# Kernel tuning notes

Hardware: AMD Instinct MI355X
Metric: run time of the kernel (lower is better)

The kernel has to match this reference:

```python
import jax, jax.numpy as jnp
import numpy as np

D_MODEL = 2048
NUM_HEADS = 16
D_H = D_MODEL // NUM_HEADS
D_LATENT = 512
B, S = 2, 2048


def setup_inputs() -> dict:
    key = jax.random.key(0)
    ks = jax.random.split(key, 10)
    sd = lambda fan_in: 1.0 / np.sqrt(fan_in)
    x = jax.random.normal(ks[0], (B, S, D_MODEL), dtype=jnp.float32)
    # weights stored as [in, out] so y = x @ W + b (same math as nn.Linear)
    w_latent = jax.random.uniform(ks[1], (D_MODEL, D_LATENT), jnp.float32, -sd(D_MODEL), sd(D_MODEL))
    b_latent = jax.random.uniform(ks[2], (D_LATENT,), jnp.float32, -sd(D_MODEL), sd(D_MODEL))
    w_q = jax.random.uniform(ks[3], (D_MODEL, D_MODEL), jnp.float32, -sd(D_MODEL), sd(D_MODEL))
    b_q = jax.random.uniform(ks[4], (D_MODEL,), jnp.float32, -sd(D_MODEL), sd(D_MODEL))
    # per-head K/V projections batched into [H, d_latent, d_h]
    w_k = jax.random.uniform(ks[5], (NUM_HEADS, D_LATENT, D_H), jnp.float32, -sd(D_LATENT), sd(D_LATENT))
    b_k = jax.random.uniform(ks[6], (NUM_HEADS, D_H), jnp.float32, -sd(D_LATENT), sd(D_LATENT))
    w_v = jax.random.uniform(ks[7], (NUM_HEADS, D_LATENT, D_H), jnp.float32, -sd(D_LATENT), sd(D_LATENT))
    b_v = jax.random.uniform(ks[8], (NUM_HEADS, D_H), jnp.float32, -sd(D_LATENT), sd(D_LATENT))
    w_o = jax.random.uniform(ks[9], (D_MODEL, D_MODEL), jnp.float32, -sd(D_MODEL), sd(D_MODEL))
    b_o = jnp.zeros((D_MODEL,), jnp.float32)
    return {"x": x, "w_latent": w_latent, "b_latent": b_latent, "w_q": w_q, "b_q": b_q,
            "w_k": w_k, "b_k": b_k, "w_v": w_v, "b_v": b_v, "w_o": w_o, "b_o": b_o}


def reference(x, w_latent, b_latent, w_q, b_q, w_k, b_k, w_v, b_v, w_o, b_o):
    batch, seq, d = x.shape
    # latent KV compression: [B,S,d_latent]
    z = x @ w_latent + b_latent
    # queries: [B,H,S,d_h]
    q = (x @ w_q + b_q).reshape(batch, seq, NUM_HEADS, D_H).transpose(0, 2, 1, 3)
    # per-head K/V projections fused into one batched GEMM: [B,H,S,d_h]
    k = jnp.einsum('bsl,hld->bhsd', z, w_k) + b_k[None, :, None, :]
    v = jnp.einsum('bsl,hld->bhsd', z, w_v) + b_v[None, :, None, :]
    attn = jnp.einsum('bhqd,bhkd->bhqk', q, k) / np.sqrt(D_H).astype(np.float32)
    attn = jax.nn.softmax(attn, axis=-1)
    out = jnp.einsum('bhqk,bhkd->bhqd', attn, v)          # [B,H,S,d_h]
    out = out.transpose(0, 2, 1, 3).reshape(batch, seq, d)  # [B,S,D]
    return out @ w_o + b_o
```

## Files before the change

kernel.cpp:

```cpp
#include <hip/hip_runtime.h>
#include <hip/hip_bf16.h>

#define H_ATT   16
#define DH      128
#define DMODEL  2048
#define DLAT    512
#define NB      2
#define SEQ     2048
#define MROWS   (NB * SEQ)
#define NQZ     (DMODEL + DLAT)
#define NKV     (2 * DMODEL)

#define SCL2 0.12751744f

typedef __bf16          bf16x8_t __attribute__((ext_vector_type(8)));
typedef float           f32x4_t  __attribute__((ext_vector_type(4)));
typedef unsigned short  u16x4_t  __attribute__((ext_vector_type(4)));

#if __has_builtin(__builtin_amdgcn_exp2f)
#define EXP2F(x) __builtin_amdgcn_exp2f(x)
#else
#define EXP2F(x) exp2f(x)
#endif

__device__ __forceinline__ unsigned short f2bf_u16(float f) {
  union { __bf16 b; unsigned short u; } cv; cv.b = (__bf16)f; return cv.u;
}

__device__ __forceinline__ void async_copy16(const __bf16* g, __bf16* l) {
  __builtin_amdgcn_global_load_lds(
      (const __attribute__((address_space(1))) unsigned int*)g,
      (__attribute__((address_space(3))) unsigned int*)l, 16, 0, 0);
}

#define NB_CAST 8192
#define NB_WQ   4096
#define NB_WL   1024
#define NB_WK   1024
#define NB_WV   1024
#define NB_WO   4096
#define NB_BIAS 26
#define NB_PREP (NB_CAST + NB_WQ + NB_WL + NB_WK + NB_WV + NB_WO + NB_BIAS)

__global__ void prep(const float* __restrict__ x,
                     const float* __restrict__ w_q, const float* __restrict__ w_latent,
                     const float* __restrict__ w_k, const float* __restrict__ w_v,
                     const float* __restrict__ w_o,
                     const float* __restrict__ b_q, const float* __restrict__ b_lat,
                     const float* __restrict__ b_k, const float* __restrict__ b_v,
                     __bf16* __restrict__ xb, __bf16* __restrict__ wqzt,
                     __bf16* __restrict__ wkvt, __bf16* __restrict__ wot,
                     float* __restrict__ bqz, float* __restrict__ bkv) {
  __shared__ float tile[32][33];
  int bi = blockIdx.x;
  int t  = threadIdx.x;

  if (bi < NB_CAST) {
    int i = bi * 256 + t;
    float4 v = ((const float4*)x)[i];
    ushort4 o;
    o.x = f2bf_u16(v.x); o.y = f2bf_u16(v.y); o.z = f2bf_u16(v.z); o.w = f2bf_u16(v.w);
    ((ushort4*)xb)[i] = o;
    return;
  }
  bi -= NB_CAST;

  const float* in = nullptr; __bf16* out = nullptr;
  int R = 0, C = 0, bx = 0, by = 0; float scale = 1.f;
  if (bi < NB_WQ) {
    in = w_q; out = wqzt; R = DMODEL; C = DMODEL; scale = SCL2;
    bx = bi & 63; by = bi >> 6;
  } else if ((bi -= NB_WQ) < NB_WL) {
    in = w_latent; out = wqzt + (size_t)DMODEL * DMODEL; R = DMODEL; C = DLAT;
    bx = bi & 15; by = bi >> 4;
  } else if ((bi -= NB_WL) < NB_WK) {
    int h = bi >> 6, rem = bi & 63;
    in = w_k + (size_t)h * DLAT * DH; out = wkvt + (size_t)h * DH * DLAT;
    R = DLAT; C = DH; bx = rem & 3; by = rem >> 2;
  } else if ((bi -= NB_WK) < NB_WV) {
    int h = bi >> 6, rem = bi & 63;
    in = w_v + (size_t)h * DLAT * DH;
    out = wkvt + (size_t)DMODEL * DLAT + (size_t)h * DH * DLAT;
    R = DLAT; C = DH; bx = rem & 3; by = rem >> 2;
  } else if ((bi -= NB_WV) < NB_WO) {
    in = w_o; out = wot; R = DMODEL; C = DMODEL;
    bx = bi & 63; by = bi >> 6;
  } else {
    bi -= NB_WO;
    int idx = bi * 256 + t;
    if (idx < DMODEL)                bqz[idx] = b_q[idx] * SCL2;
    else if (idx < NQZ)              bqz[idx] = b_lat[idx - DMODEL];
    else if (idx < NQZ + DMODEL)     bkv[idx - NQZ] = b_k[idx - NQZ];
    else if (idx < NQZ + NKV)        bkv[idx - NQZ] = b_v[idx - NQZ - DMODEL];
    return;
  }

  int tx = t & 31, ty = t >> 5;
  const float* ip = in + (size_t)(by * 32) * C + bx * 32;
  #pragma unroll
  for (int i = 0; i < 4; ++i)
    tile[ty + i * 8][tx] = ip[(size_t)(ty + i * 8) * C + tx];
  __syncthreads();
  __bf16* op = out + (size_t)(bx * 32) * R + by * 32;
  #pragma unroll
  for (int i = 0; i < 4; ++i)
    op[(size_t)(ty + i * 8) * R + tx] = (__bf16)(tile[tx][ty + i * 8] * scale);
}

#define BM 128
#define BN 128
#define BK 32

__device__ __forceinline__ void storec(float*  p, float v) { *p = v; }
__device__ __forceinline__ void storec(__bf16* p, float v) { *p = (__bf16)v; }

template <typename OutT, bool KVDUAL>
__global__ __launch_bounds__(256, 2)
void gemm_bt(const __bf16* __restrict__ A, const __bf16* __restrict__ Bt,
             const float* __restrict__ bias, OutT* __restrict__ C,
             __bf16* __restrict__ Cvt,
             int M, int N, int K, int lda, int ldc) {
  __shared__ __align__(16) __bf16 As[BM * BK];
  __shared__ __align__(16) __bf16 Bs[BN * BK];
  const int t    = threadIdx.x;
  const int wave = t >> 6, lane = t & 63;
  const int quad = lane >> 4, l16 = lane & 15;
  const int wm = (wave >> 1) * 64, wn = (wave & 1) * 64;
  const int row0 = blockIdx.y * BM, col0 = blockIdx.x * BN;
  const int srow = t >> 2, skc = t & 3;

  const __bf16* Ag  = A  + (size_t)(row0 + srow)      * lda + skc * 8;
  const __bf16* Ag2 = A  + (size_t)(row0 + srow + 64) * lda + skc * 8;
  const __bf16* Bg  = Bt + (size_t)(col0 + srow)      * K   + skc * 8;
  const __bf16* Bg2 = Bt + (size_t)(col0 + srow + 64) * K   + skc * 8;
  __bf16* Al  = As + t * 8;
  __bf16* Al2 = As + 2048 + t * 8;
  __bf16* Bl  = Bs + t * 8;
  __bf16* Bl2 = Bs + 2048 + t * 8;

  f32x4_t acc[4][4] = {};

  for (int k0 = 0; k0 < K; k0 += BK) {
    async_copy16(Ag  + k0, Al);
    async_copy16(Ag2 + k0, Al2);
    async_copy16(Bg  + k0, Bl);
    async_copy16(Bg2 + k0, Bl2);
    __syncthreads();
    bf16x8_t af[4], bfr[4];
    #pragma unroll
    for (int i = 0; i < 4; ++i)
      af[i] = *(const bf16x8_t*)(As + (wm + i * 16 + l16) * BK + quad * 8);
    #pragma unroll
    for (int j = 0; j < 4; ++j)
      bfr[j] = *(const bf16x8_t*)(Bs + (wn + j * 16 + l16) * BK + quad * 8);
    #pragma unroll
    for (int i = 0; i < 4; ++i)
      #pragma unroll
      for (int j = 0; j < 4; ++j)
        acc[i][j] = __builtin_amdgcn_mfma_f32_16x16x32_bf16(af[i], bfr[j], acc[i][j], 0, 0, 0);
    __syncthreads();
  }

  const bool vmode = KVDUAL && (col0 >= DMODEL);
  #pragma unroll
  for (int j = 0; j < 4; ++j) {
    int col = col0 + wn + j * 16 + l16;
    float bj = bias[col];
    #pragma unroll
    for (int i = 0; i < 4; ++i) {
      int row = row0 + wm + i * 16 + quad * 4;
      if (vmode) {
        u16x4_t pw;
        #pragma unroll
        for (int r = 0; r < 4; ++r) pw[r] = f2bf_u16(acc[i][j][r] + bj);
        size_t bb = (size_t)(row >> 11);
        int s = row & (SEQ - 1);
        *(u16x4_t*)(Cvt + bb * ((size_t)DMODEL * SEQ) + (size_t)(col - DMODEL) * SEQ + s) = pw;
      } else {
        #pragma unroll
        for (int r = 0; r < 4; ++r)
          storec(&C[(size_t)(row + r) * ldc + col], acc[i][j][r] + bj);
      }
    }
  }
}

#define TQ 128
#define TK 32

__global__ __launch_bounds__(256, 2)
void mla_attn(const __bf16* __restrict__ Qm, const __bf16* __restrict__ Km,
              const __bf16* __restrict__ Vtg, __bf16* __restrict__ Om) {
  __shared__ __align__(16) __bf16 Kls[2][8 * 512];
  __shared__ __align__(16) __bf16 Vls[3][8 * 512];
  __shared__ __align__(16) __bf16 Ps [2][8 * 512];
  __shared__ float Lbuf[2][TQ];

  const int t    = threadIdx.x;
  const int wave = t >> 6, lane = t & 63;
  const int quad = lane >> 4, l16 = lane & 15;
  const int wq = wave >> 1, wk = wave & 1, wd = wave & 1;
  const int h = blockIdx.y, b = blockIdx.z;
  const int q0 = blockIdx.x * TQ;
  const size_t kbase  = (size_t)b * SEQ * DMODEL + (size_t)h * DH;
  const size_t vtbase = ((size_t)b * DMODEL + (size_t)h * DH) * SEQ;
  const size_t obase  = (size_t)b * SEQ * DMODEL + (size_t)h * DH;

  bf16x8_t qf[4][4];
  #pragma unroll
  for (int nt = 0; nt < 4; ++nt) {
    const __bf16* qp = Qm + ((size_t)b * SEQ + q0 + wq * 64 + nt * 16 + l16) * NQZ
                       + (size_t)h * DH + quad * 8;
    #pragma unroll
    for (int kc = 0; kc < 4; ++kc)
      qf[nt][kc] = *(const bf16x8_t*)(qp + kc * 32);
  }

  auto stage = [&](int tile) {
    int kt0 = tile * TK;
    __bf16* Kd = Kls[tile & 1];
    __bf16* Vd = Vls[tile % 3];
    #pragma unroll
    for (int i2 = 0; i2 < 2; ++i2) {
      int bidx = wave * 2 + i2;
      int mt = bidx >> 2, kc = bidx & 3;
      async_copy16(Km + kbase + (size_t)(kt0 + mt * 16 + l16) * DMODEL + kc * 32 + quad * 8,
                   Kd + bidx * 512 + lane * 8);
      async_copy16(Vtg + vtbase + (size_t)(bidx * 16 + l16) * SEQ + kt0 + quad * 8,
                   Vd + bidx * 512 + lane * 8);
    }
  };

  f32x4_t acc_o[4][4] = {};
  float l_part[4] = {0.f, 0.f, 0.f, 0.f};

  auto pv = [&](const __bf16* Pd, const __bf16* Vd) {
    bf16x8_t pf[4];
    #pragma unroll
    for (int mq = 0; mq < 4; ++mq)
      pf[mq] = *(const bf16x8_t*)(Pd + (wq * 4 + mq) * 512 + lane * 8);
    #pragma unroll
    for (int nd = 0; nd < 4; ++nd) {
      bf16x8_t vf = *(const bf16x8_t*)(Vd + (wd * 4 + nd) * 512 + lane * 8);
      #pragma unroll
      for (int mq = 0; mq < 4; ++mq)
        acc_o[mq][nd] = __builtin_amdgcn_mfma_f32_16x16x32_bf16(pf[mq], vf, acc_o[mq][nd], 0, 0, 0);
    }
  };

  stage(0);

  for (int it = 0; it < SEQ / TK; ++it) {
    __syncthreads();
    if (it + 1 < SEQ / TK) stage(it + 1);
    if (it > 0) pv(Ps[(it - 1) & 1], Vls[(it - 1) % 3]);

    f32x4_t acc_s[4] = {};
    const __bf16* Kb = Kls[it & 1];
    #pragma unroll
    for (int kc = 0; kc < 4; ++kc) {
      bf16x8_t kf = *(const bf16x8_t*)(Kb + (wk * 4 + kc) * 512 + lane * 8);
      #pragma unroll
      for (int nt = 0; nt < 4; ++nt)
        acc_s[nt] = __builtin_amdgcn_mfma_f32_16x16x32_bf16(kf, qf[nt][kc], acc_s[nt], 0, 0, 0);
    }

    __bf16* Pd = Ps[it & 1];
    #pragma unroll
    for (int nt = 0; nt < 4; ++nt) {
      u16x4_t pw;
      float s = 0.f;
      #pragma unroll
      for (int r = 0; r < 4; ++r) {
        float p = EXP2F(fminf(acc_s[nt][r], 80.f));
        s += p;
        pw[r] = f2bf_u16(p);
      }
      l_part[nt] += s;
      *(u16x4_t*)(Pd + (wq * 4 + nt) * 512
                  + ((wk * 2 + (quad >> 1)) * 16 + l16) * 8 + (quad & 1) * 4) = pw;
    }
  }

  __syncthreads();
  pv(Ps[(SEQ / TK - 1) & 1], Vls[(SEQ / TK - 1) % 3]);

  #pragma unroll
  for (int nt = 0; nt < 4; ++nt) {
    float lp = l_part[nt];
    lp += __shfl_xor(lp, 16);
    lp += __shfl_xor(lp, 32);
    Lbuf[wk][wq * 64 + nt * 16 + l16] = lp;
  }
  __syncthreads();
  #pragma unroll
  for (int mq = 0; mq < 4; ++mq) {
    float li[4];
    #pragma unroll
    for (int r = 0; r < 4; ++r) {
      int qq = wq * 64 + mq * 16 + quad * 4 + r;
      li[r] = 1.f / (Lbuf[0][qq] + Lbuf[1][qq]);
    }
    #pragma unroll
    for (int nd = 0; nd < 4; ++nd) {
      int col = wd * 64 + nd * 16 + l16;
      #pragma unroll
      for (int r = 0; r < 4; ++r) {
        int row = q0 + wq * 64 + mq * 16 + quad * 4 + r;
        Om[obase + (size_t)row * DMODEL + col] = (__bf16)(acc_o[mq][nd][r] * li[r]);
      }
    }
  }
}

extern "C" void kernel_launch(void* const* d_in, const int* in_sizes, int n_in,
                              void* d_out, int out_size, void* d_ws, size_t ws_size,
                              hipStream_t stream) {
  (void)in_sizes; (void)n_in; (void)out_size; (void)ws_size;
  const float* x        = (const float*)d_in[0];
  const float* w_latent = (const float*)d_in[1];
  const float* b_latent = (const float*)d_in[2];
  const float* w_q      = (const float*)d_in[3];
  const float* b_q      = (const float*)d_in[4];
  const float* w_k      = (const float*)d_in[5];
  const float* b_k      = (const float*)d_in[6];
  const float* w_v      = (const float*)d_in[7];
  const float* b_v      = (const float*)d_in[8];
  const float* w_o      = (const float*)d_in[9];
  const float* b_o      = (const float*)d_in[10];
  float* out = (float*)d_out;

  __bf16* ws = (__bf16*)d_ws;
  __bf16* xb   = ws; ws += (size_t)MROWS * DMODEL;
  __bf16* wqzt = ws; ws += (size_t)NQZ * DMODEL;
  __bf16* wkvt = ws; ws += (size_t)NKV * DLAT;
  __bf16* wot  = ws; ws += (size_t)DMODEL * DMODEL;
  __bf16* qzb  = ws; ws += (size_t)MROWS * NQZ;
  __bf16* kb   = ws; ws += (size_t)MROWS * DMODEL;
  __bf16* vt   = ws; ws += (size_t)MROWS * DMODEL;
  __bf16* ao   = ws; ws += (size_t)MROWS * DMODEL;
  float*  bqz  = (float*)ws;
  float*  bkv  = bqz + NQZ;

  dim3 blk256(256);
  prep<<<NB_PREP, blk256, 0, stream>>>(x, w_q, w_latent, w_k, w_v, w_o,
                                       b_q, b_latent, b_k, b_v,
                                       xb, wqzt, wkvt, wot, bqz, bkv);

  gemm_bt<__bf16, false><<<dim3(NQZ/BN, MROWS/BM), blk256, 0, stream>>>(
      xb, wqzt, bqz, qzb, nullptr, MROWS, NQZ, DMODEL, DMODEL, NQZ);
  gemm_bt<__bf16, true><<<dim3(NKV/BN, MROWS/BM), blk256, 0, stream>>>(
      qzb + DMODEL, wkvt, bkv, kb, vt, MROWS, NKV, DLAT, NQZ, DMODEL);

  mla_attn<<<dim3(SEQ/TQ, H_ATT, NB), blk256, 0, stream>>>(qzb, kb, vt, ao);

  gemm_bt<float, false><<<dim3(DMODEL/BN, MROWS/BM), blk256, 0, stream>>>(
      ao, wot, b_o, out, nullptr, MROWS, DMODEL, DMODEL, DMODEL, DMODEL);
}
```

Baseline: 386.1 us.

## Keep softmax probabilities in registers and split keys across waves in attention

The attention kernel now uses 64-key tiles. Each wave pair splits the keys rather than the head dimension, and the bf16 probabilities feed the PV MFMA straight from registers instead of going through a shared-memory P buffer. The K rows are staged in a permuted order so the S accumulator layout matches the B-operand layout. Partial outputs from the two key-split waves are combined through shared memory at the end, with vectorized output stores. This removes the P LDS round-trip and one pipeline stage, but doubles the output accumulators to 128 floats per thread, which risks register pressure and lower occupancy.

```diff
diff --git a/kernel.cpp b/kernel.cpp
--- a/kernel.cpp
+++ b/kernel.cpp
@@ -186,20 +186,19 @@
 }
 
 #define TQ 128
-#define TK 32
+#define TK 64
+#define SMEM_BYTES 68608
+#define CMB_ST 132
 
 __global__ __launch_bounds__(256, 2)
 void mla_attn(const __bf16* __restrict__ Qm, const __bf16* __restrict__ Km,
               const __bf16* __restrict__ Vtg, __bf16* __restrict__ Om) {
-  __shared__ __align__(16) __bf16 Kls[2][8 * 512];
-  __shared__ __align__(16) __bf16 Vls[3][8 * 512];
-  __shared__ __align__(16) __bf16 Ps [2][8 * 512];
-  __shared__ float Lbuf[2][TQ];
+  __shared__ __align__(16) char smem_raw[SMEM_BYTES];
 
   const int t    = threadIdx.x;
   const int wave = t >> 6, lane = t & 63;
   const int quad = lane >> 4, l16 = lane & 15;
-  const int wq = wave >> 1, wk = wave & 1, wd = wave & 1;
+  const int wq = wave >> 1, wk = wave & 1;
   const int h = blockIdx.y, b = blockIdx.z;
   const int q0 = blockIdx.x * TQ;
   const size_t kbase  = (size_t)b * SEQ * DMODEL + (size_t)h * DH;
@@ -218,98 +217,103 @@
 
   auto stage = [&](int tile) {
     int kt0 = tile * TK;
-    __bf16* Kd = Kls[tile & 1];
-    __bf16* Vd = Vls[tile % 3];
-    #pragma unroll
-    for (int i2 = 0; i2 < 2; ++i2) {
-      int bidx = wave * 2 + i2;
-      int mt = bidx >> 2, kc = bidx & 3;
-      async_copy16(Km + kbase + (size_t)(kt0 + mt * 16 + l16) * DMODEL + kc * 32 + quad * 8,
+    __bf16* Kd = (__bf16*)smem_raw + (tile & 1) * 8192;
+    __bf16* Vd = (__bf16*)smem_raw + 16384 + (tile & 1) * 8192;
+    #pragma unroll
+    for (int i2 = 0; i2 < 4; ++i2) {
+      int bidx = wave * 4 + i2;
+      int wk2 = bidx >> 3, mt = (bidx >> 2) & 1, kc = bidx & 3;
+      int keyrow = kt0 + wk2 * 32 + (l16 >> 2) * 8 + mt * 4 + (l16 & 3);
+      async_copy16(Km + kbase + (size_t)keyrow * DMODEL + kc * 32 + quad * 8,
                    Kd + bidx * 512 + lane * 8);
-      async_copy16(Vtg + vtbase + (size_t)(bidx * 16 + l16) * SEQ + kt0 + quad * 8,
+      int dt = bidx & 7;
+      async_copy16(Vtg + vtbase + (size_t)(dt * 16 + l16) * SEQ + kt0 + wk2 * 32 + quad * 8,
                    Vd + bidx * 512 + lane * 8);
     }
   };
 
-  f32x4_t acc_o[4][4] = {};
+  f32x4_t acc_o[8][4] = {};
   float l_part[4] = {0.f, 0.f, 0.f, 0.f};
-
-  auto pv = [&](const __bf16* Pd, const __bf16* Vd) {
-    bf16x8_t pf[4];
-    #pragma unroll
-    for (int mq = 0; mq < 4; ++mq)
-      pf[mq] = *(const bf16x8_t*)(Pd + (wq * 4 + mq) * 512 + lane * 8);
-    #pragma unroll
-    for (int nd = 0; nd < 4; ++nd) {
-      bf16x8_t vf = *(const bf16x8_t*)(Vd + (wd * 4 + nd) * 512 + lane * 8);
-      #pragma unroll
-      for (int mq = 0; mq < 4; ++mq)
-        acc_o[mq][nd] = __builtin_amdgcn_mfma_f32_16x16x32_bf16(pf[mq], vf, acc_o[mq][nd], 0, 0, 0);
-    }
-  };
 
   stage(0);
 
   for (int it = 0; it < SEQ / TK; ++it) {
     __syncthreads();
     if (it + 1 < SEQ / TK) stage(it + 1);
-    if (it > 0) pv(Ps[(it - 1) & 1], Vls[(it - 1) % 3]);
-
-    f32x4_t acc_s[4] = {};
-    const __bf16* Kb = Kls[it & 1];
-    #pragma unroll
-    for (int kc = 0; kc < 4; ++kc) {
-      bf16x8_t kf = *(const bf16x8_t*)(Kb + (wk * 4 + kc) * 512 + lane * 8);
+    const __bf16* Kb = (const __bf16*)smem_raw + (it & 1) * 8192;
+    const __bf16* Vb = (const __bf16*)smem_raw + 16384 + (it & 1) * 8192;
+
+    union { bf16x8_t v8; unsigned short u[8]; } pfr[4];
+    #pragma unroll
+    for (int mt = 0; mt < 2; ++mt) {
+      f32x4_t acc_s[4] = {};
+      #pragma unroll
+      for (int kc = 0; kc < 4; ++kc) {
+        bf16x8_t kf = *(const bf16x8_t*)(Kb + ((wk * 2 + mt) * 4 + kc) * 512 + lane * 8);
+        #pragma unroll
+        for (int nt = 0; nt < 4; ++nt)
+          acc_s[nt] = __builtin_amdgcn_mfma_f32_16x16x32_bf16(kf, qf[nt][kc], acc_s[nt], 0, 0, 0);
+      }
+      #pragma unroll
+      for (int nt = 0; nt < 4; ++nt) {
+        float s = 0.f;
+        #pragma unroll
+        for (int r = 0; r < 4; ++r) {
+          float p = EXP2F(fminf(acc_s[nt][r], 80.f));
+          s += p;
+          pfr[nt].u[mt * 4 + r] = f2bf_u16(p);
+        }
+        l_part[nt] += s;
+      }
+    }
+
+    #pragma unroll
+    for (int dt = 0; dt < 8; ++dt) {
+      bf16x8_t vf = *(const bf16x8_t*)(Vb + (wk * 8 + dt) * 512 + lane * 8);
       #pragma unroll
       for (int nt = 0; nt < 4; ++nt)
-        acc_s[nt] = __builtin_amdgcn_mfma_f32_16x16x32_bf16(kf, qf[nt][kc], acc_s[nt], 0, 0, 0);
-    }
-
-    __bf16* Pd = Ps[it & 1];
-    #pragma unroll
-    for (int nt = 0; nt < 4; ++nt) {
-      u16x4_t pw;
-      float s = 0.f;
-      #pragma unroll
-      for (int r = 0; r < 4; ++r) {
-        float p = EXP2F(fminf(acc_s[nt][r], 80.f));
-        s += p;
-        pw[r] = f2bf_u16(p);
-      }
-      l_part[nt] += s;
-      *(u16x4_t*)(Pd + (wq * 4 + nt) * 512
-                  + ((wk * 2 + (quad >> 1)) * 16 + l16) * 8 + (quad & 1) * 4) = pw;
-    }
-  }
-
-  __syncthreads();
-  pv(Ps[(SEQ / TK - 1) & 1], Vls[(SEQ / TK - 1) % 3]);
-
+        acc_o[dt][nt] = __builtin_amdgcn_mfma_f32_16x16x32_bf16(vf, pfr[nt].v8, acc_o[dt][nt], 0, 0, 0);
+    }
+  }
+
+  float* Lb = (float*)(smem_raw + 67584);
   #pragma unroll
   for (int nt = 0; nt < 4; ++nt) {
     float lp = l_part[nt];
     lp += __shfl_xor(lp, 16);
     lp += __shfl_xor(lp, 32);
-    Lbuf[wk][wq * 64 + nt * 16 + l16] = lp;
+    Lb[wk * 128 + wq * 64 + nt * 16 + l16] = lp;
   }
   __syncthreads();
-  #pragma unroll
-  for (int mq = 0; mq < 4; ++mq) {
-    float li[4];
-    #pragma unroll
-    for (int r = 0; r < 4; ++r) {
-      int qq = wq * 64 + mq * 16 + quad * 4 + r;
-      li[r] = 1.f / (Lbuf[0][qq] + Lbuf[1][qq]);
-    }
-    #pragma unroll
-    for (int nd = 0; nd < 4; ++nd) {
-      int col = wd * 64 + nd * 16 + l16;
-      #pragma unroll
-      for (int r = 0; r < 4; ++r) {
-        int row = q0 + wq * 64 + mq * 16 + quad * 4 + r;
-        Om[obase + (size_t)row * DMODEL + col] = (__bf16)(acc_o[mq][nd][r] * li[r]);
+
+  float* Cmb = (float*)smem_raw + (size_t)wq * 64 * CMB_ST;
+  if (wk) {
+    #pragma unroll
+    for (int dt = 0; dt < 8; ++dt)
+      #pragma unroll
+      for (int nt = 0; nt < 4; ++nt)
+        *(f32x4_t*)(Cmb + (nt * 16 + l16) * CMB_ST + dt * 16 + quad * 4) = acc_o[dt][nt];
+  }
+  __syncthreads();
+  if (!wk) {
+    float linv[4];
+    #pragma unroll
+    for (int nt = 0; nt < 4; ++nt) {
+      int qq = wq * 64 + nt * 16 + l16;
+      linv[nt] = 1.f / (Lb[qq] + Lb[128 + qq]);
+    }
+    #pragma unroll
+    for (int dt = 0; dt < 8; ++dt)
+      #pragma unroll
+      for (int nt = 0; nt < 4; ++nt) {
+        f32x4_t o = *(const f32x4_t*)(Cmb + (nt * 16 + l16) * CMB_ST + dt * 16 + quad * 4);
+        u16x4_t st;
+        #pragma unroll
+        for (int r = 0; r < 4; ++r)
+          st[r] = f2bf_u16((acc_o[dt][nt][r] + o[r]) * linv[nt]);
+        *(u16x4_t*)(Om + obase + (size_t)(q0 + wq * 64 + nt * 16 + l16) * DMODEL
+                    + dt * 16 + quad * 4) = st;
       }
-    }
   }
 }
 
```

New measurement: 369.8 us. 4.2% less time.

## Double key tile to 64 and remap attention blocks so each XCD shares heads

Applied to the files above, without the earlier changes.

Increases the attention key tile from 32 to 64 and restructures the LDS pipeline to single K and P buffers with a double-buffered V, adding a second barrier per iteration. The aim is to halve the number of loop iterations and barriers while doing more MFMA work per iteration. It also swaps the 3D grid for a 1D grid whose block index is remapped so blocks of the same head and batch land on the same XCD, improving L2 reuse of K and V. The extra barrier reduces overlap between the async copies and compute, and larger register tiles may pressure occupancy.

```diff
diff --git a/kernel.cpp b/kernel.cpp
--- a/kernel.cpp
+++ b/kernel.cpp
@@ -186,22 +186,25 @@
 }
 
 #define TQ 128
-#define TK 32
+#define TK 64
 
 __global__ __launch_bounds__(256, 2)
 void mla_attn(const __bf16* __restrict__ Qm, const __bf16* __restrict__ Km,
               const __bf16* __restrict__ Vtg, __bf16* __restrict__ Om) {
-  __shared__ __align__(16) __bf16 Kls[2][8 * 512];
-  __shared__ __align__(16) __bf16 Vls[3][8 * 512];
-  __shared__ __align__(16) __bf16 Ps [2][8 * 512];
+  __shared__ __align__(16) __bf16 Kls[16 * 512];
+  __shared__ __align__(16) __bf16 Vls[2][16 * 512];
+  __shared__ __align__(16) __bf16 Ps [16 * 512];
   __shared__ float Lbuf[2][TQ];
 
   const int t    = threadIdx.x;
   const int wave = t >> 6, lane = t & 63;
   const int quad = lane >> 4, l16 = lane & 15;
   const int wq = wave >> 1, wk = wave & 1, wd = wave & 1;
-  const int h = blockIdx.y, b = blockIdx.z;
-  const int q0 = blockIdx.x * TQ;
+  const int lin  = blockIdx.x;
+  const int xcd  = lin & 7, slot = lin >> 3;
+  const int hb   = xcd * 4 + (slot >> 4);
+  const int b    = hb >> 4, h = hb & 15;
+  const int q0   = (slot & 15) * TQ;
   const size_t kbase  = (size_t)b * SEQ * DMODEL + (size_t)h * DH;
   const size_t vtbase = ((size_t)b * DMODEL + (size_t)h * DH) * SEQ;
   const size_t obase  = (size_t)b * SEQ * DMODEL + (size_t)h * DH;
@@ -216,74 +219,102 @@
       qf[nt][kc] = *(const bf16x8_t*)(qp + kc * 32);
   }
 
-  auto stage = [&](int tile) {
-    int kt0 = tile * TK;
-    __bf16* Kd = Kls[tile & 1];
-    __bf16* Vd = Vls[tile % 3];
-    #pragma unroll
-    for (int i2 = 0; i2 < 2; ++i2) {
-      int bidx = wave * 2 + i2;
+  auto stage = [&](int kt0, int vbuf) {
+    #pragma unroll
+    for (int i2 = 0; i2 < 4; ++i2) {
+      int bidx = wave * 4 + i2;
       int mt = bidx >> 2, kc = bidx & 3;
       async_copy16(Km + kbase + (size_t)(kt0 + mt * 16 + l16) * DMODEL + kc * 32 + quad * 8,
-                   Kd + bidx * 512 + lane * 8);
-      async_copy16(Vtg + vtbase + (size_t)(bidx * 16 + l16) * SEQ + kt0 + quad * 8,
-                   Vd + bidx * 512 + lane * 8);
+                   Kls + bidx * 512 + lane * 8);
+      int dt = bidx >> 1, ks = bidx & 1;
+      async_copy16(Vtg + vtbase + (size_t)(dt * 16 + l16) * SEQ + kt0 + ks * 32 + quad * 8,
+                   Vls[vbuf] + bidx * 512 + lane * 8);
     }
   };
 
   f32x4_t acc_o[4][4] = {};
   float l_part[4] = {0.f, 0.f, 0.f, 0.f};
 
-  auto pv = [&](const __bf16* Pd, const __bf16* Vd) {
-    bf16x8_t pf[4];
-    #pragma unroll
-    for (int mq = 0; mq < 4; ++mq)
-      pf[mq] = *(const bf16x8_t*)(Pd + (wq * 4 + mq) * 512 + lane * 8);
-    #pragma unroll
-    for (int nd = 0; nd < 4; ++nd) {
-      bf16x8_t vf = *(const bf16x8_t*)(Vd + (wd * 4 + nd) * 512 + lane * 8);
-      #pragma unroll
-      for (int mq = 0; mq < 4; ++mq)
-        acc_o[mq][nd] = __builtin_amdgcn_mfma_f32_16x16x32_bf16(pf[mq], vf, acc_o[mq][nd], 0, 0, 0);
-    }
-  };
-
-  stage(0);
-
+  stage(0, 0);
+
+  f32x4_t acc_s[2][4];
   for (int it = 0; it < SEQ / TK; ++it) {
     __syncthreads();
-    if (it + 1 < SEQ / TK) stage(it + 1);
-    if (it > 0) pv(Ps[(it - 1) & 1], Vls[(it - 1) % 3]);
-
-    f32x4_t acc_s[4] = {};
-    const __bf16* Kb = Kls[it & 1];
-    #pragma unroll
-    for (int kc = 0; kc < 4; ++kc) {
-      bf16x8_t kf = *(const bf16x8_t*)(Kb + (wk * 4 + kc) * 512 + lane * 8);
+
+    if (it > 0) {
+      const __bf16* Vb = Vls[(it - 1) & 1];
+      #pragma unroll
+      for (int ks = 0; ks < 2; ++ks) {
+        bf16x8_t pf[4];
+        #pragma unroll
+        for (int mq = 0; mq < 4; ++mq)
+          pf[mq] = *(const bf16x8_t*)(Ps + ((wq * 4 + mq) * 2 + ks) * 512 + lane * 8);
+        #pragma unroll
+        for (int nd = 0; nd < 4; ++nd) {
+          bf16x8_t vf = *(const bf16x8_t*)(Vb + ((wd * 4 + nd) * 2 + ks) * 512 + lane * 8);
+          #pragma unroll
+          for (int mq = 0; mq < 4; ++mq)
+            acc_o[mq][nd] = __builtin_amdgcn_mfma_f32_16x16x32_bf16(pf[mq], vf, acc_o[mq][nd], 0, 0, 0);
+        }
+      }
+    }
+
+    #pragma unroll
+    for (int mtl = 0; mtl < 2; ++mtl)
       #pragma unroll
       for (int nt = 0; nt < 4; ++nt)
-        acc_s[nt] = __builtin_amdgcn_mfma_f32_16x16x32_bf16(kf, qf[nt][kc], acc_s[nt], 0, 0, 0);
-    }
-
-    __bf16* Pd = Ps[it & 1];
+        acc_s[mtl][nt] = f32x4_t{0.f, 0.f, 0.f, 0.f};
+    #pragma unroll
+    for (int kc = 0; kc < 4; ++kc)
+      #pragma unroll
+      for (int mtl = 0; mtl < 2; ++mtl) {
+        bf16x8_t kf = *(const bf16x8_t*)(Kls + ((wk * 2 + mtl) * 4 + kc) * 512 + lane * 8);
+        #pragma unroll
+        for (int nt = 0; nt < 4; ++nt)
+          acc_s[mtl][nt] = __builtin_amdgcn_mfma_f32_16x16x32_bf16(kf, qf[nt][kc], acc_s[mtl][nt], 0, 0, 0);
+      }
+
+    __syncthreads();
+
+    if (it + 1 < SEQ / TK) stage((it + 1) * TK, (it + 1) & 1);
+
     #pragma unroll
     for (int nt = 0; nt < 4; ++nt) {
-      u16x4_t pw;
-      float s = 0.f;
-      #pragma unroll
-      for (int r = 0; r < 4; ++r) {
-        float p = EXP2F(fminf(acc_s[nt][r], 80.f));
-        s += p;
-        pw[r] = f2bf_u16(p);
-      }
-      l_part[nt] += s;
-      *(u16x4_t*)(Pd + (wq * 4 + nt) * 512
-                  + ((wk * 2 + (quad >> 1)) * 16 + l16) * 8 + (quad & 1) * 4) = pw;
+      #pragma unroll
+      for (int mtl = 0; mtl < 2; ++mtl) {
+        u16x4_t pw;
+        float s = 0.f;
+        #pragma unroll
+        for (int r = 0; r < 4; ++r) {
+          float p = EXP2F(fminf(acc_s[mtl][nt][r], 80.f));
+          s += p;
+          pw[r] = f2bf_u16(p);
+        }
+        l_part[nt] += s;
+        *(u16x4_t*)(Ps + ((wq * 4 + nt) * 2 + wk) * 512
+                    + ((mtl * 2 + (quad >> 1)) * 16 + l16) * 8 + (quad & 1) * 4) = pw;
+      }
     }
   }
 
   __syncthreads();
-  pv(Ps[(SEQ / TK - 1) & 1], Vls[(SEQ / TK - 1) % 3]);
+  {
+    const __bf16* Vb = Vls[(SEQ / TK - 1) & 1];
+    #pragma unroll
+    for (int ks = 0; ks < 2; ++ks) {
+      bf16x8_t pf[4];
+      #pragma unroll
+      for (int mq = 0; mq < 4; ++mq)
+        pf[mq] = *(const bf16x8_t*)(Ps + ((wq * 4 + mq) * 2 + ks) * 512 + lane * 8);
+      #pragma unroll
+      for (int nd = 0; nd < 4; ++nd) {
+        bf16x8_t vf = *(const bf16x8_t*)(Vb + ((wd * 4 + nd) * 2 + ks) * 512 + lane * 8);
+        #pragma unroll
+        for (int mq = 0; mq < 4; ++mq)
+          acc_o[mq][nd] = __builtin_amdgcn_mfma_f32_16x16x32_bf16(pf[mq], vf, acc_o[mq][nd], 0, 0, 0);
+      }
+    }
+  }
 
   #pragma unroll
   for (int nt = 0; nt < 4; ++nt) {
@@ -352,7 +383,7 @@
   gemm_bt<__bf16, true><<<dim3(NKV/BN, MROWS/BM), blk256, 0, stream>>>(
       qzb + DMODEL, wkvt, bkv, kb, vt, MROWS, NKV, DLAT, NQZ, DMODEL);
 
-  mla_attn<<<dim3(SEQ/TQ, H_ATT, NB), blk256, 0, stream>>>(qzb, kb, vt, ao);
+  mla_attn<<<dim3(512), blk256, 0, stream>>>(qzb, kb, vt, ao);
 
   gemm_bt<float, false><<<dim3(DMODEL/BN, MROWS/BM), blk256, 0, stream>>>(
       ao, wot, b_o, out, nullptr, MROWS, DMODEL, DMODEL, DMODEL, DMODEL);
```

Result: faster. 344.4 us (-10.8%).
